# Kernel tuning notes

Measured on AMD Instinct MI355X. Metric: run time of the kernel, lower is better.

The kernel has to match this reference:

```python
import jax, jax.numpy as jnp
import numpy as np

IN_SIZE = 64
NUM_FEATURES = 32
NUM_HEADS = 8
EPS = 1e-5


def setup_inputs() -> dict:
    key = jax.random.key(0)
    ks = jax.random.split(key, 12)
    D, F, Hh = IN_SIZE, NUM_FEATURES, NUM_HEADS
    M = Hh * F  # MLP width = num_heads * num_features
    s = 0.05
    return {
        "x": jax.random.normal(ks[0], (2, D, 48, 48), dtype=jnp.float32),
        # stacked per-head projection weights, stored [in, out]
        "Wq": jax.random.normal(ks[1], (Hh, D, F), dtype=jnp.float32) * s,
        "bq": jax.random.normal(ks[2], (Hh, F), dtype=jnp.float32) * s,
        "Wk": jax.random.normal(ks[3], (Hh, D, F), dtype=jnp.float32) * s,
        "bk": jax.random.normal(ks[4], (Hh, F), dtype=jnp.float32) * s,
        "Wv": jax.random.normal(ks[5], (Hh, D, F), dtype=jnp.float32) * s,
        "bv": jax.random.normal(ks[6], (Hh, F), dtype=jnp.float32) * s,
        "W1": jax.random.normal(ks[7], (M, M), dtype=jnp.float32) * s,
        "b1": jax.random.normal(ks[8], (M,), dtype=jnp.float32) * s,
        "W2": jax.random.normal(ks[9], (M, M), dtype=jnp.float32) * s,
        "b2": jax.random.normal(ks[10], (M,), dtype=jnp.float32) * s,
        "gamma": jnp.ones((M,), dtype=jnp.float32),
        "beta": jnp.zeros((M,), dtype=jnp.float32),
    }


def _inorm_lastdim(y):
    # InstanceNorm1d applied to channels-last tensor: normalizes LAST dim,
    # biased variance, eps=1e-5, no affine.
    mu = jnp.mean(y, axis=-1, keepdims=True)
    var = jnp.mean(jnp.square(y - mu), axis=-1, keepdims=True)
    return (y - mu) / jnp.sqrt(var + EPS)


def reference(x, Wq, bq, Wk, bk, Wv, bv, W1, b1, W2, b2, gamma, beta):
    N, D, H, W = x.shape
    F = NUM_FEATURES
    L = H * W
    flat = jnp.transpose(x, (0, 2, 3, 1)).reshape(N, L, D)  # [N, L, D]

    def proj(Wm, bm):  # Wm [Hh, D, F], bm [Hh, F] -> [Hh, N, L, F]
        y = jnp.einsum('nld,hdf->hnlf', flat, Wm) + bm[:, None, None, :]
        return jax.nn.relu(_inorm_lastdim(y))

    Q = proj(Wq, bq)
    K = proj(Wk, bk)
    V = proj(Wv, bv)

    scores = jnp.einsum('hnlf,hnmf->hnlm', Q, K) / jnp.sqrt(jnp.float32(F))
    # original: F.softmax(scaled) on 3D [N,L,L] -> legacy dim=1 (first L axis)
    att = jax.nn.softmax(scores, axis=2)
    A = jnp.einsum('hnlm,hnmf->hnlf', att, V)  # [Hh, N, L, F]

    heads = jnp.transpose(A, (1, 2, 0, 3)).reshape(N, L, NUM_HEADS * F)
    m = jax.nn.relu(heads @ W1 + b1)
    m = jax.nn.relu(m @ W2 + b2)
    o = _inorm_lastdim(m + heads)
    o = gamma * o + beta  # [N, L, Hh*F]
    return jnp.transpose(o, (0, 2, 1)).reshape(N, NUM_HEADS * F, H, W)
```

## Files before the change

kernel.cpp:

```cpp
#include <hip/hip_runtime.h>
#include <hip/hip_bf16.h>
#include <stdint.h>

#define L_TOT 2304
#define D_IN  64
#define NF    32
#define NH    8
#define NB    2
#define MW    256
#define CHS   8
#define NSTRIP (L_TOT/32)
#define RT    32

constexpr float EPSV  = 1e-5f;
constexpr float SCALE2 = 0.2550351f;

typedef __bf16  bf16x8  __attribute__((ext_vector_type(8)));
typedef float   f32x16  __attribute__((ext_vector_type(16)));

union U32x4BF { uint32_t u[4]; bf16x8 v; };

static __device__ __forceinline__ uint32_t pack_bf16(float a, float b) {
    union { __bf16 h[2]; uint32_t u; } r;
    r.h[0] = (__bf16)a;
    r.h[1] = (__bf16)b;
    return r.u;
}

__global__ __launch_bounds__(256) void k_prep(
    const float* __restrict__ x,
    const float* __restrict__ Wq, const float* __restrict__ Wk, const float* __restrict__ Wv,
    const float* __restrict__ W1, const float* __restrict__ W2,
    __hip_bfloat16* __restrict__ xb, __hip_bfloat16* __restrict__ Wqkvt,
    __hip_bfloat16* __restrict__ W1t, __hip_bfloat16* __restrict__ W2t)
{
    const int job = blockIdx.x;
    const int tx = threadIdx.x & 31, ty = threadIdx.x >> 5;
    __shared__ float t[64][33];

    if (job < 128) {
        const int z = job >> 6;
        const int tt = job & 63;
        const int bi = (tt >> 3) * 32, bj = (tt & 7) * 32;
        const float* src = z ? W2 : W1;
        __hip_bfloat16* dst = z ? W2t : W1t;
        #pragma unroll
        for (int k = 0; k < 4; ++k)
            t[ty + 8 * k][tx] = src[(size_t)(bi + ty + 8 * k) * MW + bj + tx];
        __syncthreads();
        #pragma unroll
        for (int k = 0; k < 4; ++k)
            dst[(size_t)(bj + ty + 8 * k) * MW + bi + tx] =
                __float2bfloat16(t[tx][ty + 8 * k]);
        return;
    }

    const float* src;
    size_t sstride;
    __hip_bfloat16* dst;
    if (job < 152) {
        int j = job - 128;
        int mtx = j >> 3, h = j & 7;
        const float* Wm = mtx == 0 ? Wq : (mtx == 1 ? Wk : Wv);
        src = Wm + (size_t)h * D_IN * NF;
        sstride = NF;
        dst = Wqkvt + (size_t)j * NF * D_IN;
    } else {
        int i = job - 152;
        int n = i / NSTRIP, lt = i % NSTRIP;
        src = x + (size_t)n * D_IN * L_TOT + lt * 32;
        sstride = L_TOT;
        dst = xb + ((size_t)n * L_TOT + lt * 32) * D_IN;
    }
    #pragma unroll
    for (int k = 0; k < 8; ++k)
        t[ty + 8 * k][tx] = src[(size_t)(ty + 8 * k) * sstride + tx];
    __syncthreads();
    #pragma unroll
    for (int k = 0; k < 4; ++k) {
        int col = ty + 8 * k;
        #pragma unroll
        for (int j = 0; j < 2; ++j)
            dst[(size_t)col * D_IN + tx + 32 * j] = __float2bfloat16(t[tx + 32 * j][col]);
    }
}

__global__ __launch_bounds__(256) void k_proj(
    const __hip_bfloat16* __restrict__ xb, const __hip_bfloat16* __restrict__ Wqkvt,
    const float* __restrict__ bq, const float* __restrict__ bk, const float* __restrict__ bv,
    __hip_bfloat16* __restrict__ Qo, __hip_bfloat16* __restrict__ Ko,
    __hip_bfloat16* __restrict__ Vt)
{
    const int ltile = blockIdx.x;
    const int n = blockIdx.y;
    const int h = blockIdx.z * 4 + (threadIdx.x >> 6);
    const int l0 = ltile * 32;
    const int lane = threadIdx.x & 63;
    const int c = lane & 31, hi = lane >> 5;
    const int hn = h * NB + n;

    const bf16x8* xp = reinterpret_cast<const bf16x8*>(
        xb + ((size_t)n * L_TOT + l0 + c) * D_IN);
    bf16x8 xf[4];
    #pragma unroll
    for (int t = 0; t < 4; ++t) xf[t] = xp[2 * t + hi];

    const float* bs[3] = {bq, bk, bv};

    #pragma unroll
    for (int mtx = 0; mtx < 3; ++mtx) {
        const bf16x8* wp = reinterpret_cast<const bf16x8*>(
            Wqkvt + ((size_t)(mtx * NH + h) * NF + c) * D_IN);
        f32x16 acc = {};
        #pragma unroll
        for (int t = 0; t < 4; ++t)
            acc = __builtin_amdgcn_mfma_f32_32x32x16_bf16(wp[2 * t + hi], xf[t], acc, 0, 0, 0);

        float bb[16];
        #pragma unroll
        for (int g = 0; g < 4; ++g) {
            float4 t4 = *reinterpret_cast<const float4*>(&bs[mtx][h * NF + 8 * g + 4 * hi]);
            bb[4 * g + 0] = t4.x; bb[4 * g + 1] = t4.y;
            bb[4 * g + 2] = t4.z; bb[4 * g + 3] = t4.w;
        }

        float v[16], s = 0.f, s2 = 0.f;
        #pragma unroll
        for (int r = 0; r < 16; ++r) {
            v[r] = acc[r] + bb[r];
            s += v[r]; s2 += v[r] * v[r];
        }
        s  += __shfl_xor(s, 32, 64);
        s2 += __shfl_xor(s2, 32, 64);
        float mu = s * (1.f / 32);
        float rstd = rsqrtf(s2 * (1.f / 32) - mu * mu + EPSV);
        float y[16];
        #pragma unroll
        for (int r = 0; r < 16; ++r) y[r] = fmaxf((v[r] - mu) * rstd, 0.f);

        if (mtx == 2) {
            #pragma unroll
            for (int r = 0; r < 16; ++r) {
                int f = (r & 3) + 8 * (r >> 2) + 4 * hi;
                Vt[((size_t)(hn * NSTRIP + ltile) * NF + f) * 32 + c] = __float2bfloat16(y[r]);
            }
        } else {
            if (mtx == 0) {
                #pragma unroll
                for (int r = 0; r < 16; ++r) y[r] *= SCALE2;
            }
            uint32_t pk[8];
            #pragma unroll
            for (int q = 0; q < 8; ++q) pk[q] = pack_bf16(y[2 * q], y[2 * q + 1]);
            uint32_t rr[4];
            #pragma unroll
            for (int j = 0; j < 4; ++j)
                rr[j] = (uint32_t)__shfl_xor((int)(hi ? pk[j] : pk[4 + j]), 32, 64);
            uint32_t row[8];
            if (hi == 0) {
                row[0] = pk[0]; row[1] = pk[1]; row[2] = rr[0]; row[3] = rr[1];
                row[4] = pk[2]; row[5] = pk[3]; row[6] = rr[2]; row[7] = rr[3];
            } else {
                row[0] = rr[0]; row[1] = rr[1]; row[2] = pk[4]; row[3] = pk[5];
                row[4] = rr[2]; row[5] = rr[3]; row[6] = pk[6]; row[7] = pk[7];
            }
            __hip_bfloat16* dst = (mtx == 0 ? Qo : Ko)
                + ((size_t)hn * L_TOT + l0 + c) * NF + hi * 16;
            reinterpret_cast<uint4*>(dst)[0] = make_uint4(row[0], row[1], row[2], row[3]);
            reinterpret_cast<uint4*>(dst)[1] = make_uint4(row[4], row[5], row[6], row[7]);
        }
    }
}

__global__ __launch_bounds__(256) void k_stats(
    const __hip_bfloat16* __restrict__ Qb, const __hip_bfloat16* __restrict__ Kb,
    float* __restrict__ zpart)
{
    const int w = threadIdx.x >> 6;
    const int strip = blockIdx.x * 4 + w;
    const int hn = blockIdx.y;
    const int chunk = blockIdx.z;
    const int lane = threadIdx.x & 63;
    const int c = lane & 31, hi = lane >> 5;

    const bf16x8* kp = reinterpret_cast<const bf16x8*>(
        Kb + ((size_t)hn * L_TOT + strip * 32 + c) * NF);
    const bf16x8 ka0 = kp[hi];
    const bf16x8 ka1 = kp[2 + hi];

    float Zr[16];
    #pragma unroll
    for (int r = 0; r < 16; ++r) Zr[r] = 0.f;

    for (int it = 0; it < (L_TOT / 32) / CHS; ++it) {
        const int l0 = (chunk * ((L_TOT / 32) / CHS) + it) * 32;
        const bf16x8* qp = reinterpret_cast<const bf16x8*>(
            Qb + ((size_t)hn * L_TOT + l0 + c) * NF);
        bf16x8 qb0 = qp[hi];
        bf16x8 qb1 = qp[2 + hi];
        f32x16 s16 = {};
        s16 = __builtin_amdgcn_mfma_f32_32x32x16_bf16(ka0, qb0, s16, 0, 0, 0);
        s16 = __builtin_amdgcn_mfma_f32_32x32x16_bf16(ka1, qb1, s16, 0, 0, 0);
        #pragma unroll
        for (int r = 0; r < 16; ++r) Zr[r] += exp2f(s16[r]);
    }
    #pragma unroll
    for (int r = 0; r < 16; ++r) {
        #pragma unroll
        for (int o = 16; o >= 1; o >>= 1) Zr[r] += __shfl_xor(Zr[r], o, 64);
    }
    if (c == 0) {
        float4* zp = reinterpret_cast<float4*>(
            zpart + ((size_t)chunk * 16 + hn) * L_TOT + strip * 32 + hi * 16);
        zp[0] = make_float4(Zr[0], Zr[1], Zr[2], Zr[3]);
        zp[1] = make_float4(Zr[4], Zr[5], Zr[6], Zr[7]);
        zp[2] = make_float4(Zr[8], Zr[9], Zr[10], Zr[11]);
        zp[3] = make_float4(Zr[12], Zr[13], Zr[14], Zr[15]);
    }
}

__global__ __launch_bounds__(256) void k_norm(
    const float* __restrict__ zpart, __hip_bfloat16* __restrict__ Vt)
{
    const int strip = blockIdx.x, hn = blockIdx.y;
    __shared__ float zs[CHS][32];
    __shared__ float zinv_s[32];

    const int cc = threadIdx.x >> 5, p = threadIdx.x & 31;
    zs[cc][p] = zpart[((size_t)cc * 16 + hn) * L_TOT + strip * 32 + p];
    __syncthreads();
    if (threadIdx.x < 32) {
        const int p2 = threadIdx.x;
        float Z = 0.f;
        #pragma unroll
        for (int k = 0; k < CHS; ++k) Z += zs[k][p2];
        const int hi = p2 >> 4, r = p2 & 15;
        const int m_local = (r & 3) + 8 * (r >> 2) + 4 * hi;
        zinv_s[m_local] = 1.f / Z;
    }
    __syncthreads();

    const int f = threadIdx.x >> 3, mg = (threadIdx.x & 7) * 4;
    __hip_bfloat16* pv = Vt + ((size_t)(hn * NSTRIP + strip) * NF + f) * 32 + mg;
    uint2* p2v = reinterpret_cast<uint2*>(pv);
    union { uint2 u2; __bf16 h[4]; } in, outv;
    in.u2 = *p2v;
    outv.h[0] = (__bf16)((float)in.h[0] * zinv_s[mg + 0]);
    outv.h[1] = (__bf16)((float)in.h[1] * zinv_s[mg + 1]);
    outv.h[2] = (__bf16)((float)in.h[2] * zinv_s[mg + 2]);
    outv.h[3] = (__bf16)((float)in.h[3] * zinv_s[mg + 3]);
    *p2v = outv.u2;
}

static __device__ __forceinline__ void apply_strip(
    int st, int hn, const bf16x8& qb0, const bf16x8& qb1,
    const __hip_bfloat16* __restrict__ Kb, const __hip_bfloat16* __restrict__ Vt,
    int c, int hi, f32x16& acc)
{
    const bf16x8* kp = reinterpret_cast<const bf16x8*>(
        Kb + ((size_t)hn * L_TOT + st * 32 + c) * NF);
    f32x16 s16 = {};
    s16 = __builtin_amdgcn_mfma_f32_32x32x16_bf16(kp[hi], qb0, s16, 0, 0, 0);
    s16 = __builtin_amdgcn_mfma_f32_32x32x16_bf16(kp[2 + hi], qb1, s16, 0, 0, 0);

    float p[16];
    #pragma unroll
    for (int r = 0; r < 16; ++r) p[r] = exp2f(s16[r]);

    uint32_t wp[8];
    #pragma unroll
    for (int q = 0; q < 8; ++q) wp[q] = pack_bf16(p[2 * q], p[2 * q + 1]);

    uint32_t sendA = hi ? wp[0] : wp[2];
    uint32_t sendB = hi ? wp[1] : wp[3];
    uint32_t rA = (uint32_t)__shfl_xor((int)sendA, 32, 64);
    uint32_t rB = (uint32_t)__shfl_xor((int)sendB, 32, 64);
    U32x4BF fragP0;
    fragP0.u[0] = hi ? rA    : wp[0];
    fragP0.u[1] = hi ? rB    : wp[1];
    fragP0.u[2] = hi ? wp[2] : rA;
    fragP0.u[3] = hi ? wp[3] : rB;
    uint32_t sendC = hi ? wp[4] : wp[6];
    uint32_t sendD = hi ? wp[5] : wp[7];
    uint32_t rC = (uint32_t)__shfl_xor((int)sendC, 32, 64);
    uint32_t rD = (uint32_t)__shfl_xor((int)sendD, 32, 64);
    U32x4BF fragP1;
    fragP1.u[0] = hi ? rC    : wp[4];
    fragP1.u[1] = hi ? rD    : wp[5];
    fragP1.u[2] = hi ? wp[6] : rC;
    fragP1.u[3] = hi ? wp[7] : rD;

    const bf16x8* vp = reinterpret_cast<const bf16x8*>(
        Vt + ((size_t)(hn * NSTRIP + st) * NF + c) * 32);
    acc = __builtin_amdgcn_mfma_f32_32x32x16_bf16(fragP0.v, vp[hi], acc, 0, 0, 0);
    acc = __builtin_amdgcn_mfma_f32_32x32x16_bf16(fragP1.v, vp[2 + hi], acc, 0, 0, 0);
}

__global__ __launch_bounds__(512) void k_apply(
    const __hip_bfloat16* __restrict__ Qb, const __hip_bfloat16* __restrict__ Kb,
    const __hip_bfloat16* __restrict__ Vt,
    float* __restrict__ partA)
{
    const int w = threadIdx.x >> 6;
    const int ltile = blockIdx.x;
    const int l0 = ltile * 32;
    const int hn = blockIdx.y;
    const int lane = threadIdx.x & 63;
    const int c = lane & 31, hi = lane >> 5;

    const bf16x8* qp = reinterpret_cast<const bf16x8*>(
        Qb + ((size_t)hn * L_TOT + l0 + c) * NF);
    const bf16x8 qb0 = qp[hi];
    const bf16x8 qb1 = qp[2 + hi];

    f32x16 accA = {}, accB = {};
    const int sbase = w * (NSTRIP / 8);
    #pragma unroll
    for (int it2 = 0; it2 < 4; ++it2) {
        apply_strip(sbase + 2 * it2,     hn, qb0, qb1, Kb, Vt, c, hi, accA);
        apply_strip(sbase + 2 * it2 + 1, hn, qb0, qb1, Kb, Vt, c, hi, accB);
    }
    apply_strip(sbase + 8, hn, qb0, qb1, Kb, Vt, c, hi, accA);

    __shared__ float red[8][16][64];
    #pragma unroll
    for (int r = 0; r < 16; ++r) red[w][r][lane] = accA[r] + accB[r];
    __syncthreads();

    const int n = hn & 1, h = hn >> 1;
    float* outp = partA + ((size_t)(n * L_TOT + l0)) * MW + h * NF + c;
    #pragma unroll
    for (int j = 0; j < 2; ++j) {
        const int r = 2 * w + j;
        float sv = 0.f;
        #pragma unroll
        for (int k = 0; k < 8; ++k) sv += red[k][r][lane];
        const int row = (r & 3) + 8 * (r >> 2) + 4 * hi;
        outp[(size_t)row * MW] = sv;
    }
}

__global__ __launch_bounds__(512) void k_mlp(
    const float* __restrict__ partA,
    const __hip_bfloat16* __restrict__ W1t, const float* __restrict__ b1,
    const __hip_bfloat16* __restrict__ W2t, const float* __restrict__ b2,
    const float* __restrict__ gamma, const float* __restrict__ beta,
    float* __restrict__ out)
{
    const int blk = blockIdx.x;
    const int n  = blk / (L_TOT / RT);
    const int l0 = (blk % (L_TOT / RT)) * RT;
    const int tid = threadIdx.x;
    const int w = tid >> 6, lane = tid & 63;
    const int c = lane & 31, hi = lane >> 5;
    const int n0 = w * 32;

    __shared__ __align__(16) char smem[67584];
    float (*hsf)[MW] = reinterpret_cast<float (*)[MW]>(smem);
    __hip_bfloat16 (*hA)[264]  = reinterpret_cast<__hip_bfloat16 (*)[264]>(smem + 32768);
    __hip_bfloat16 (*msb)[264] = reinterpret_cast<__hip_bfloat16 (*)[264]>(smem + 49664);
    float (*ys)[MW] = reinterpret_cast<float (*)[MW]>(smem + 32768);
    float (*rs)[4]  = reinterpret_cast<float (*)[4]>(smem + 66560);
    float (*rs2)[4] = reinterpret_cast<float (*)[4]>(smem + 67072);

    for (int idx = tid; idx < RT * MW; idx += 512) {
        int r = idx >> 8, i = idx & 255;
        float v = partA[((size_t)n * L_TOT + l0 + r) * MW + i];
        hsf[r][i] = v;
        hA[r][i] = __float2bfloat16(v);
    }
    __syncthreads();

    const float bb1 = b1[n0 + c];
    bf16x8 B1[16];
    #pragma unroll
    for (int k0 = 0; k0 < 16; ++k0)
        B1[k0] = *reinterpret_cast<const bf16x8*>(W1t + (size_t)(n0 + c) * MW + k0 * 16 + hi * 8);
    f32x16 a1 = {}, a1b = {};
    #pragma unroll
    for (int k0 = 0; k0 < 8; ++k0) {
        bf16x8 ae = *reinterpret_cast<const bf16x8*>(&hA[c][(2 * k0) * 16 + hi * 8]);
        bf16x8 ao = *reinterpret_cast<const bf16x8*>(&hA[c][(2 * k0 + 1) * 16 + hi * 8]);
        a1  = __builtin_amdgcn_mfma_f32_32x32x16_bf16(ae, B1[2 * k0],     a1,  0, 0, 0);
        a1b = __builtin_amdgcn_mfma_f32_32x32x16_bf16(ao, B1[2 * k0 + 1], a1b, 0, 0, 0);
    }
    #pragma unroll
    for (int r = 0; r < 16; ++r) {
        int row = (r & 3) + 8 * (r >> 2) + 4 * hi;
        msb[row][n0 + c] = __float2bfloat16(fmaxf(a1[r] + a1b[r] + bb1, 0.f));
    }
    __syncthreads();

    const float bb2 = b2[n0 + c];
    bf16x8 B2[16];
    #pragma unroll
    for (int k0 = 0; k0 < 16; ++k0)
        B2[k0] = *reinterpret_cast<const bf16x8*>(W2t + (size_t)(n0 + c) * MW + k0 * 16 + hi * 8);
    f32x16 a2 = {}, a2b = {};
    #pragma unroll
    for (int k0 = 0; k0 < 8; ++k0) {
        bf16x8 ae = *reinterpret_cast<const bf16x8*>(&msb[c][(2 * k0) * 16 + hi * 8]);
        bf16x8 ao = *reinterpret_cast<const bf16x8*>(&msb[c][(2 * k0 + 1) * 16 + hi * 8]);
        a2  = __builtin_amdgcn_mfma_f32_32x32x16_bf16(ae, B2[2 * k0],     a2,  0, 0, 0);
        a2b = __builtin_amdgcn_mfma_f32_32x32x16_bf16(ao, B2[2 * k0 + 1], a2b, 0, 0, 0);
    }
    float yv[16];
    #pragma unroll
    for (int r = 0; r < 16; ++r) {
        int row = (r & 3) + 8 * (r >> 2) + 4 * hi;
        yv[r] = fmaxf(a2[r] + a2b[r] + bb2, 0.f) + hsf[row][n0 + c];
    }
    __syncthreads();
    #pragma unroll
    for (int r = 0; r < 16; ++r) {
        int row = (r & 3) + 8 * (r >> 2) + 4 * hi;
        ys[row][n0 + c] = yv[r];
    }
    __syncthreads();

    const int col = tid & 255;
    const int half = tid >> 8;
    const int wid = (tid >> 6) & 3;
    float vv[16];
    #pragma unroll
    for (int r = 0; r < 16; ++r) {
        float v = ys[half * 16 + r][col];
        vv[r] = v;
        float s = v, s2 = v * v;
        #pragma unroll
        for (int o = 32; o >= 1; o >>= 1) { s += __shfl_xor(s, o, 64); s2 += __shfl_xor(s2, o, 64); }
        if (lane == 0) { rs[half * 16 + r][wid] = s; rs2[half * 16 + r][wid] = s2; }
    }
    __syncthreads();
    const float g = gamma[col], be = beta[col];
    float ov[16];
    #pragma unroll
    for (int r = 0; r < 16; ++r) {
        int row = half * 16 + r;
        float s  = rs[row][0]  + rs[row][1]  + rs[row][2]  + rs[row][3];
        float s2 = rs2[row][0] + rs2[row][1] + rs2[row][2] + rs2[row][3];
        float mu  = s  * (1.f / MW);
        float var = s2 * (1.f / MW) - mu * mu;
        ov[r] = g * ((vv[r] - mu) * rsqrtf(var + EPSV)) + be;
    }
    float* ob = out + ((size_t)n * MW + col) * L_TOT + l0 + half * 16;
    #pragma unroll
    for (int q = 0; q < 4; ++q)
        reinterpret_cast<float4*>(ob)[q] =
            make_float4(ov[4 * q], ov[4 * q + 1], ov[4 * q + 2], ov[4 * q + 3]);
}

extern "C" void kernel_launch(void* const* d_in, const int* in_sizes, int n_in,
                              void* d_out, int out_size, void* d_ws, size_t ws_size,
                              hipStream_t stream) {
    const float* x  = (const float*)d_in[0];
    const float* Wq = (const float*)d_in[1];
    const float* bq = (const float*)d_in[2];
    const float* Wk = (const float*)d_in[3];
    const float* bk = (const float*)d_in[4];
    const float* Wv = (const float*)d_in[5];
    const float* bv = (const float*)d_in[6];
    const float* W1 = (const float*)d_in[7];
    const float* b1 = (const float*)d_in[8];
    const float* W2 = (const float*)d_in[9];
    const float* b2 = (const float*)d_in[10];
    const float* gm = (const float*)d_in[11];
    const float* bt = (const float*)d_in[12];
    float* out = (float*)d_out;

    const size_t QKVE = (size_t)16 * L_TOT * NF;
    const size_t XBE  = (size_t)NB * L_TOT * D_IN;
    const size_t WQE  = (size_t)3 * NH * NF * D_IN;
    const size_t WTE  = (size_t)MW * MW;
    const size_t ZN = (size_t)CHS * 16 * L_TOT;

    __hip_bfloat16* Qb = (__hip_bfloat16*)d_ws;
    __hip_bfloat16* Kb = Qb + QKVE;
    __hip_bfloat16* Vt = Kb + QKVE;
    __hip_bfloat16* xb = Vt + QKVE;
    __hip_bfloat16* Wqkvt = xb + XBE;
    __hip_bfloat16* W1t = Wqkvt + WQE;
    __hip_bfloat16* W2t = W1t + WTE;
    float* zpart = (float*)(W2t + WTE);
    float* partA = zpart + ZN;

    k_prep<<<dim3(296), dim3(256), 0, stream>>>(
        x, Wq, Wk, Wv, W1, W2, xb, Wqkvt, W1t, W2t);
    k_proj<<<dim3(NSTRIP, NB, 2), dim3(256), 0, stream>>>(
        xb, Wqkvt, bq, bk, bv, Qb, Kb, Vt);
    k_stats<<<dim3(NSTRIP / 4, 16, CHS), dim3(256), 0, stream>>>(Qb, Kb, zpart);
    k_norm<<<dim3(NSTRIP, 16), dim3(256), 0, stream>>>(zpart, Vt);
    k_apply<<<dim3(NSTRIP, 16), dim3(512), 0, stream>>>(Qb, Kb, Vt, partA);
    k_mlp<<<dim3(NB * (L_TOT / RT)), dim3(512), 0, stream>>>(
        partA, W1t, b1, W2t, b2, gm, bt, out);
}
```

Measured before the change: 121.0 us.

## Shrink MLP row tile to 16 with 16x16 MFMA and simplify softmax stats reduction

The MLP kernel now processes 16 rows per block instead of 32, using 16x16x32 bf16 MFMAs with weights streamed from global memory instead of register-cached. That doubles the grid and cuts shared memory for more parallelism and occupancy, at the cost of reading the weights twice as often. The stats kernel swaps the MFMA operand order, so each lane accumulates its column's softmax denominator directly. This replaces the 16-register cross-lane shuffle reduction with a single shuffle and plain stores, and the norm kernel drops the row remapping to match.

```diff
diff --git a/kernel.cpp b/kernel.cpp
--- a/kernel.cpp
+++ b/kernel.cpp
@@ -10,13 +10,13 @@
 #define MW    256
 #define CHS   8
 #define NSTRIP (L_TOT/32)
-#define RT    32
 
 constexpr float EPSV  = 1e-5f;
 constexpr float SCALE2 = 0.2550351f;
 
 typedef __bf16  bf16x8  __attribute__((ext_vector_type(8)));
 typedef float   f32x16  __attribute__((ext_vector_type(16)));
+typedef float   f32x4   __attribute__((ext_vector_type(4)));
 
 union U32x4BF { uint32_t u[4]; bf16x8 v; };
 
@@ -185,38 +185,31 @@
 
     const bf16x8* kp = reinterpret_cast<const bf16x8*>(
         Kb + ((size_t)hn * L_TOT + strip * 32 + c) * NF);
-    const bf16x8 ka0 = kp[hi];
-    const bf16x8 ka1 = kp[2 + hi];
-
-    float Zr[16];
-    #pragma unroll
-    for (int r = 0; r < 16; ++r) Zr[r] = 0.f;
+    const bf16x8 kb0 = kp[hi];
+    const bf16x8 kb1 = kp[2 + hi];
+
+    float z0 = 0.f, z1 = 0.f, z2 = 0.f, z3 = 0.f;
 
     for (int it = 0; it < (L_TOT / 32) / CHS; ++it) {
         const int l0 = (chunk * ((L_TOT / 32) / CHS) + it) * 32;
         const bf16x8* qp = reinterpret_cast<const bf16x8*>(
             Qb + ((size_t)hn * L_TOT + l0 + c) * NF);
-        bf16x8 qb0 = qp[hi];
-        bf16x8 qb1 = qp[2 + hi];
         f32x16 s16 = {};
-        s16 = __builtin_amdgcn_mfma_f32_32x32x16_bf16(ka0, qb0, s16, 0, 0, 0);
-        s16 = __builtin_amdgcn_mfma_f32_32x32x16_bf16(ka1, qb1, s16, 0, 0, 0);
-        #pragma unroll
-        for (int r = 0; r < 16; ++r) Zr[r] += exp2f(s16[r]);
-    }
-    #pragma unroll
-    for (int r = 0; r < 16; ++r) {
-        #pragma unroll
-        for (int o = 16; o >= 1; o >>= 1) Zr[r] += __shfl_xor(Zr[r], o, 64);
-    }
-    if (c == 0) {
-        float4* zp = reinterpret_cast<float4*>(
-            zpart + ((size_t)chunk * 16 + hn) * L_TOT + strip * 32 + hi * 16);
-        zp[0] = make_float4(Zr[0], Zr[1], Zr[2], Zr[3]);
-        zp[1] = make_float4(Zr[4], Zr[5], Zr[6], Zr[7]);
-        zp[2] = make_float4(Zr[8], Zr[9], Zr[10], Zr[11]);
-        zp[3] = make_float4(Zr[12], Zr[13], Zr[14], Zr[15]);
-    }
+        s16 = __builtin_amdgcn_mfma_f32_32x32x16_bf16(qp[hi], kb0, s16, 0, 0, 0);
+        s16 = __builtin_amdgcn_mfma_f32_32x32x16_bf16(qp[2 + hi], kb1, s16, 0, 0, 0);
+        #pragma unroll
+        for (int r = 0; r < 4; ++r) z0 += exp2f(s16[r]);
+        #pragma unroll
+        for (int r = 4; r < 8; ++r) z1 += exp2f(s16[r]);
+        #pragma unroll
+        for (int r = 8; r < 12; ++r) z2 += exp2f(s16[r]);
+        #pragma unroll
+        for (int r = 12; r < 16; ++r) z3 += exp2f(s16[r]);
+    }
+    float Z = (z0 + z1) + (z2 + z3);
+    Z += __shfl_xor(Z, 32, 64);
+    if (hi == 0)
+        zpart[((size_t)chunk * 16 + hn) * L_TOT + strip * 32 + c] = Z;
 }
 
 __global__ __launch_bounds__(256) void k_norm(
@@ -230,13 +223,10 @@
     zs[cc][p] = zpart[((size_t)cc * 16 + hn) * L_TOT + strip * 32 + p];
     __syncthreads();
     if (threadIdx.x < 32) {
-        const int p2 = threadIdx.x;
         float Z = 0.f;
         #pragma unroll
-        for (int k = 0; k < CHS; ++k) Z += zs[k][p2];
-        const int hi = p2 >> 4, r = p2 & 15;
-        const int m_local = (r & 3) + 8 * (r >> 2) + 4 * hi;
-        zinv_s[m_local] = 1.f / Z;
+        for (int k = 0; k < CHS; ++k) Z += zs[k][threadIdx.x];
+        zinv_s[threadIdx.x] = 1.f / Z;
     }
     __syncthreads();
 
@@ -348,22 +338,23 @@
     float* __restrict__ out)
 {
     const int blk = blockIdx.x;
-    const int n  = blk / (L_TOT / RT);
-    const int l0 = (blk % (L_TOT / RT)) * RT;
+    const int n  = blk / (L_TOT / 16);
+    const int l0 = (blk % (L_TOT / 16)) * 16;
     const int tid = threadIdx.x;
     const int w = tid >> 6, lane = tid & 63;
-    const int c = lane & 31, hi = lane >> 5;
+    const int ar = lane & 15;
+    const int kg = lane >> 4;
     const int n0 = w * 32;
 
-    __shared__ __align__(16) char smem[67584];
+    __shared__ __align__(16) char smem[50176];
     float (*hsf)[MW] = reinterpret_cast<float (*)[MW]>(smem);
-    __hip_bfloat16 (*hA)[264]  = reinterpret_cast<__hip_bfloat16 (*)[264]>(smem + 32768);
-    __hip_bfloat16 (*msb)[264] = reinterpret_cast<__hip_bfloat16 (*)[264]>(smem + 49664);
-    float (*ys)[MW] = reinterpret_cast<float (*)[MW]>(smem + 32768);
-    float (*rs)[4]  = reinterpret_cast<float (*)[4]>(smem + 66560);
-    float (*rs2)[4] = reinterpret_cast<float (*)[4]>(smem + 67072);
-
-    for (int idx = tid; idx < RT * MW; idx += 512) {
+    __hip_bfloat16 (*hA)[264]  = reinterpret_cast<__hip_bfloat16 (*)[264]>(smem + 16384);
+    __hip_bfloat16 (*msb)[264] = reinterpret_cast<__hip_bfloat16 (*)[264]>(smem + 24832);
+    float (*ys)[MW] = reinterpret_cast<float (*)[MW]>(smem + 33280);
+    float (*rs)[4]  = reinterpret_cast<float (*)[4]>(smem + 49664);
+    float (*rs2)[4] = reinterpret_cast<float (*)[4]>(smem + 49920);
+
+    for (int idx = tid; idx < 16 * MW; idx += 512) {
         int r = idx >> 8, i = idx & 255;
         float v = partA[((size_t)n * L_TOT + l0 + r) * MW + i];
         hsf[r][i] = v;
@@ -371,83 +362,82 @@
     }
     __syncthreads();
 
-    const float bb1 = b1[n0 + c];
-    bf16x8 B1[16];
-    #pragma unroll
-    for (int k0 = 0; k0 < 16; ++k0)
-        B1[k0] = *reinterpret_cast<const bf16x8*>(W1t + (size_t)(n0 + c) * MW + k0 * 16 + hi * 8);
-    f32x16 a1 = {}, a1b = {};
-    #pragma unroll
-    for (int k0 = 0; k0 < 8; ++k0) {
-        bf16x8 ae = *reinterpret_cast<const bf16x8*>(&hA[c][(2 * k0) * 16 + hi * 8]);
-        bf16x8 ao = *reinterpret_cast<const bf16x8*>(&hA[c][(2 * k0 + 1) * 16 + hi * 8]);
-        a1  = __builtin_amdgcn_mfma_f32_32x32x16_bf16(ae, B1[2 * k0],     a1,  0, 0, 0);
-        a1b = __builtin_amdgcn_mfma_f32_32x32x16_bf16(ao, B1[2 * k0 + 1], a1b, 0, 0, 0);
-    }
-    #pragma unroll
-    for (int r = 0; r < 16; ++r) {
-        int row = (r & 3) + 8 * (r >> 2) + 4 * hi;
-        msb[row][n0 + c] = __float2bfloat16(fmaxf(a1[r] + a1b[r] + bb1, 0.f));
-    }
-    __syncthreads();
-
-    const float bb2 = b2[n0 + c];
-    bf16x8 B2[16];
-    #pragma unroll
-    for (int k0 = 0; k0 < 16; ++k0)
-        B2[k0] = *reinterpret_cast<const bf16x8*>(W2t + (size_t)(n0 + c) * MW + k0 * 16 + hi * 8);
-    f32x16 a2 = {}, a2b = {};
-    #pragma unroll
-    for (int k0 = 0; k0 < 8; ++k0) {
-        bf16x8 ae = *reinterpret_cast<const bf16x8*>(&msb[c][(2 * k0) * 16 + hi * 8]);
-        bf16x8 ao = *reinterpret_cast<const bf16x8*>(&msb[c][(2 * k0 + 1) * 16 + hi * 8]);
-        a2  = __builtin_amdgcn_mfma_f32_32x32x16_bf16(ae, B2[2 * k0],     a2,  0, 0, 0);
-        a2b = __builtin_amdgcn_mfma_f32_32x32x16_bf16(ao, B2[2 * k0 + 1], a2b, 0, 0, 0);
-    }
-    float yv[16];
-    #pragma unroll
-    for (int r = 0; r < 16; ++r) {
-        int row = (r & 3) + 8 * (r >> 2) + 4 * hi;
-        yv[r] = fmaxf(a2[r] + a2b[r] + bb2, 0.f) + hsf[row][n0 + c];
-    }
-    __syncthreads();
-    #pragma unroll
-    for (int r = 0; r < 16; ++r) {
-        int row = (r & 3) + 8 * (r >> 2) + 4 * hi;
-        ys[row][n0 + c] = yv[r];
+    f32x4 acc0 = {}, acc1 = {};
+    {
+        const __hip_bfloat16* B0p = W1t + (size_t)(n0 + ar) * MW + kg * 8;
+        const __hip_bfloat16* B1p = W1t + (size_t)(n0 + 16 + ar) * MW + kg * 8;
+        #pragma unroll
+        for (int ks = 0; ks < 8; ++ks) {
+            bf16x8 a  = *reinterpret_cast<const bf16x8*>(&hA[ar][ks * 32 + kg * 8]);
+            bf16x8 b0 = *reinterpret_cast<const bf16x8*>(B0p + ks * 32);
+            bf16x8 b1v = *reinterpret_cast<const bf16x8*>(B1p + ks * 32);
+            acc0 = __builtin_amdgcn_mfma_f32_16x16x32_bf16(a, b0, acc0, 0, 0, 0);
+            acc1 = __builtin_amdgcn_mfma_f32_16x16x32_bf16(a, b1v, acc1, 0, 0, 0);
+        }
+    }
+    {
+        const float bb0 = b1[n0 + ar], bb1 = b1[n0 + 16 + ar];
+        #pragma unroll
+        for (int r = 0; r < 4; ++r) {
+            int row = kg * 4 + r;
+            msb[row][n0 + ar]      = __float2bfloat16(fmaxf(acc0[r] + bb0, 0.f));
+            msb[row][n0 + 16 + ar] = __float2bfloat16(fmaxf(acc1[r] + bb1, 0.f));
+        }
+    }
+    __syncthreads();
+
+    f32x4 a20 = {}, a21 = {};
+    {
+        const __hip_bfloat16* B0p = W2t + (size_t)(n0 + ar) * MW + kg * 8;
+        const __hip_bfloat16* B1p = W2t + (size_t)(n0 + 16 + ar) * MW + kg * 8;
+        #pragma unroll
+        for (int ks = 0; ks < 8; ++ks) {
+            bf16x8 a  = *reinterpret_cast<const bf16x8*>(&msb[ar][ks * 32 + kg * 8]);
+            bf16x8 b0 = *reinterpret_cast<const bf16x8*>(B0p + ks * 32);
+            bf16x8 b1v = *reinterpret_cast<const bf16x8*>(B1p + ks * 32);
+            a20 = __builtin_amdgcn_mfma_f32_16x16x32_bf16(a, b0, a20, 0, 0, 0);
+            a21 = __builtin_amdgcn_mfma_f32_16x16x32_bf16(a, b1v, a21, 0, 0, 0);
+        }
+    }
+    {
+        const float bb0 = b2[n0 + ar], bb1 = b2[n0 + 16 + ar];
+        #pragma unroll
+        for (int r = 0; r < 4; ++r) {
+            int row = kg * 4 + r;
+            ys[row][n0 + ar]      = fmaxf(a20[r] + bb0, 0.f) + hsf[row][n0 + ar];
+            ys[row][n0 + 16 + ar] = fmaxf(a21[r] + bb1, 0.f) + hsf[row][n0 + 16 + ar];
+        }
     }
     __syncthreads();
 
     const int col = tid & 255;
     const int half = tid >> 8;
     const int wid = (tid >> 6) & 3;
-    float vv[16];
-    #pragma unroll
-    for (int r = 0; r < 16; ++r) {
-        float v = ys[half * 16 + r][col];
+    float vv[8];
+    #pragma unroll
+    for (int r = 0; r < 8; ++r) {
+        float v = ys[half * 8 + r][col];
         vv[r] = v;
         float s = v, s2 = v * v;
         #pragma unroll
         for (int o = 32; o >= 1; o >>= 1) { s += __shfl_xor(s, o, 64); s2 += __shfl_xor(s2, o, 64); }
-        if (lane == 0) { rs[half * 16 + r][wid] = s; rs2[half * 16 + r][wid] = s2; }
+        if (lane == 0) { rs[half * 8 + r][wid] = s; rs2[half * 8 + r][wid] = s2; }
     }
     __syncthreads();
     const float g = gamma[col], be = beta[col];
-    float ov[16];
-    #pragma unroll
-    for (int r = 0; r < 16; ++r) {
-        int row = half * 16 + r;
+    float ov[8];
+    #pragma unroll
+    for (int r = 0; r < 8; ++r) {
+        int row = half * 8 + r;
         float s  = rs[row][0]  + rs[row][1]  + rs[row][2]  + rs[row][3];
         float s2 = rs2[row][0] + rs2[row][1] + rs2[row][2] + rs2[row][3];
         float mu  = s  * (1.f / MW);
         float var = s2 * (1.f / MW) - mu * mu;
         ov[r] = g * ((vv[r] - mu) * rsqrtf(var + EPSV)) + be;
     }
-    float* ob = out + ((size_t)n * MW + col) * L_TOT + l0 + half * 16;
-    #pragma unroll
-    for (int q = 0; q < 4; ++q)
-        reinterpret_cast<float4*>(ob)[q] =
-            make_float4(ov[4 * q], ov[4 * q + 1], ov[4 * q + 2], ov[4 * q + 3]);
+    float* ob = out + ((size_t)n * MW + col) * L_TOT + l0 + half * 8;
+    reinterpret_cast<float4*>(ob)[0] = make_float4(ov[0], ov[1], ov[2], ov[3]);
+    reinterpret_cast<float4*>(ob)[1] = make_float4(ov[4], ov[5], ov[6], ov[7]);
 }
 
 extern "C" void kernel_launch(void* const* d_in, const int* in_sizes, int n_in,
@@ -491,6 +481,6 @@
     k_stats<<<dim3(NSTRIP / 4, 16, CHS), dim3(256), 0, stream>>>(Qb, Kb, zpart);
     k_norm<<<dim3(NSTRIP, 16), dim3(256), 0, stream>>>(zpart, Vt);
     k_apply<<<dim3(NSTRIP, 16), dim3(512), 0, stream>>>(Qb, Kb, Vt, partA);
-    k_mlp<<<dim3(NB * (L_TOT / RT)), dim3(512), 0, stream>>>(
+    k_mlp<<<dim3(NB * (L_TOT / 16)), dim3(512), 0, stream>>>(
         partA, W1t, b1, W2t, b2, gm, bt, out);
 }
```

Result: slower. 123.9 us (+2.4%).
